# Optimization experiments

Hardware: AMD Instinct MI355X
Metric: run time of the kernel (lower is better)

## Reference

```python
import jax, jax.numpy as jnp
import numpy as np

N = 50000   # nodes
E = 800000  # edges per relation (avg degree 16)
IN = 128    # input feature dim
H = 2       # attention heads per layer
OUT = 64    # output feats per head
R = 2       # number of relations
NEG_SLOPE = 0.2


def _edge_softmax(e, dst, n):
    # e: [E, H] edge scores; softmax over incoming edges of each dst node
    m = jax.ops.segment_max(e, dst, num_segments=n)  # [N, H]
    m = jnp.where(jnp.isfinite(m), m, 0.0)
    ex = jnp.exp(e - jax.lax.stop_gradient(m)[dst])
    s = jax.ops.segment_sum(ex, dst, num_segments=n)  # [N, H]
    return ex / s[dst]


def _gat_layer(h, W, al, ar, b, src, dst):
    # h: [N, in]; W: [R, in, H*OUT]; al/ar: [R, H, OUT]; b: [R, H*OUT]
    # src/dst: [R, E] int32. HeteroGraphConv with sum aggregation over relations.
    acc = jnp.zeros((N, H, OUT), h.dtype)
    for r in range(R):  # small fixed relation count
        f = (h @ W[r]).reshape(N, H, OUT)           # projected feats
        el = (f * al[r]).sum(-1)                    # [N, H]
        er = (f * ar[r]).sum(-1)                    # [N, H]
        e = jax.nn.leaky_relu(el[src[r]] + er[dst[r]], NEG_SLOPE)  # [E, H]
        a = _edge_softmax(e, dst[r], N)             # [E, H]
        msg = f[src[r]] * a[:, :, None]             # [E, H, OUT]
        agg = jax.ops.segment_sum(msg, dst[r], num_segments=N)     # [N, H, OUT]
        acc = acc + jax.nn.elu(agg + b[r].reshape(1, H, OUT))
    return acc.reshape(N, H * OUT)  # flatten(1)


def setup_inputs() -> dict:
    key = jax.random.key(0)
    k = jax.random.split(key, 13)
    s = 0.05
    f32 = jnp.float32
    return {
        "x": jax.random.normal(k[0], (N, IN), f32),
        "W0": jax.random.normal(k[1], (R, IN, H * OUT), f32) * s,
        "al0": jax.random.normal(k[2], (R, H, OUT), f32) * s,
        "ar0": jax.random.normal(k[3], (R, H, OUT), f32) * s,
        "b0": jax.random.normal(k[4], (R, H * OUT), f32) * s,
        "W1": jax.random.normal(k[5], (R, H * OUT, H * OUT), f32) * s,
        "al1": jax.random.normal(k[6], (R, H, OUT), f32) * s,
        "ar1": jax.random.normal(k[7], (R, H, OUT), f32) * s,
        "b1": jax.random.normal(k[8], (R, H * OUT), f32) * s,
        "src0": jax.random.randint(k[9], (R, E), 0, N, jnp.int32),
        "dst0": jax.random.randint(k[10], (R, E), 0, N, jnp.int32),
        "src1": jax.random.randint(k[11], (R, E), 0, N, jnp.int32),
        "dst1": jax.random.randint(k[12], (R, E), 0, N, jnp.int32),
    }


def reference(x, W0, al0, ar0, b0, W1, al1, ar1, b1, src0, dst0, src1, dst1):
    h = _gat_layer(x, W0, al0, ar0, b0, src0, dst0)  # [N, H*OUT]
    h = _gat_layer(h, W1, al1, ar1, b1, src1, dst1)  # [N, H*OUT]
    return h
```

## Files before the change

kernel.cpp:

```cpp
#include <hip/hip_runtime.h>

#define NN 50000
#define NE 800000
#define DIM 128
#define NB 128
#define CH 4096
#define CAP 8192

typedef unsigned int uint;
typedef unsigned short ushort;
typedef __attribute__((ext_vector_type(8))) short v8s;
typedef __attribute__((ext_vector_type(4))) float v4f;

__device__ __forceinline__ ushort f2bf(float f) {
    union { float f; uint i; } c; c.f = f;
    const uint r = (c.i + 0x7fffu + ((c.i >> 16) & 1u)) >> 16;
    return (ushort)r;
}

__global__ __launch_bounds__(256) void conv_wt(
    const float* __restrict__ W0, const float* __restrict__ W1,
    ushort* __restrict__ WT)
{
    const int t = blockIdx.x * 256 + threadIdx.x;
#pragma unroll
    for (int i = 0; i < 4; i++) {
        const int o = t * 4 + i;
        const int m = o >> 14, rem = o & 16383;
        const int nrow = rem >> 7, k = rem & 127;
        const float* src = (m < 2) ? (W0 + (size_t)m * 16384)
                                   : (W1 + (size_t)(m - 2) * 16384);
        WT[o] = f2bf(src[k * 128 + nrow]);
    }
}

__global__ __launch_bounds__(256) void gemm_dual(
    const ushort* __restrict__ hbf, const float* __restrict__ xf,
    const ushort* __restrict__ WT,
    const float* __restrict__ al, const float* __restrict__ ar,
    ushort* __restrict__ fg0, ushort* __restrict__ fg1,
    float* __restrict__ elb, int n, int is_f32)
{
    __shared__ ushort tile[64][136];
    const int tid = threadIdx.x;
    const int w = tid >> 6, lane = tid & 63;
    const int quad = lane >> 4, l16 = lane & 15;
    const int row0 = blockIdx.x * 64 + w * 16;

    int arow = row0 + l16;
    if (arow >= n) arow = n - 1;

    v8s afr[4];
    if (is_f32) {
        const float* ap = xf + (size_t)arow * DIM + quad * 8;
#pragma unroll
        for (int kt = 0; kt < 4; kt++) {
            const float4 a0 = *(const float4*)(ap + kt * 32);
            const float4 a1 = *(const float4*)(ap + kt * 32 + 4);
            ushort tmp[8] = { f2bf(a0.x), f2bf(a0.y), f2bf(a0.z), f2bf(a0.w),
                              f2bf(a1.x), f2bf(a1.y), f2bf(a1.z), f2bf(a1.w) };
            afr[kt] = *(const v8s*)tmp;
        }
    } else {
        const ushort* ap = hbf + (size_t)arow * DIM + quad * 8;
#pragma unroll
        for (int kt = 0; kt < 4; kt++) afr[kt] = *(const v8s*)(ap + kt * 32);
    }

    for (int rel = 0; rel < 2; rel++) {
        const ushort* bp = WT + (size_t)rel * DIM * DIM + (size_t)l16 * DIM + quad * 8;
        v4f acc[8];
#pragma unroll
        for (int nt = 0; nt < 8; nt++) acc[nt] = (v4f)0.0f;
#pragma unroll
        for (int kt = 0; kt < 4; kt++) {
#pragma unroll
            for (int nt = 0; nt < 8; nt++) {
                const v8s b = *(const v8s*)(bp + (size_t)nt * 16 * DIM + kt * 32);
                acc[nt] = __builtin_amdgcn_mfma_f32_16x16x32_bf16(afr[kt], b, acc[nt], 0, 0, 0);
            }
        }

        const float* alr = al + rel * DIM;
        const float* arr = ar + rel * DIM;
        float pel[4][2], per2[4][2];
#pragma unroll
        for (int r = 0; r < 4; r++)
            pel[r][0] = pel[r][1] = per2[r][0] = per2[r][1] = 0.f;
#pragma unroll
        for (int nt = 0; nt < 8; nt++) {
            const int col = nt * 16 + l16;
            const float av = alr[col], rv = arr[col];
            const int head = nt >> 2;
#pragma unroll
            for (int r = 0; r < 4; r++) {
                pel[r][head] += acc[nt][r] * av;
                per2[r][head] += acc[nt][r] * rv;
            }
        }
#pragma unroll
        for (int o = 1; o < 16; o <<= 1) {
#pragma unroll
            for (int r = 0; r < 4; r++) {
#pragma unroll
                for (int h = 0; h < 2; h++) {
                    pel[r][h] += __shfl_xor(pel[r][h], o);
                    per2[r][h] += __shfl_xor(per2[r][h], o);
                }
            }
        }
        float* elp = elb + (size_t)rel * NN * 4;
        float* erp = elp + (size_t)NN * 2;
        if (l16 == 0) {
#pragma unroll
            for (int r = 0; r < 4; r++) {
                const int row = row0 + quad * 4 + r;
                if (row < n) {
#pragma unroll
                    for (int h = 0; h < 2; h++) {
                        elp[row * 2 + h] = pel[r][h];
                        erp[row * 2 + h] = per2[r][h];
                    }
                }
            }
        }

        __syncthreads();
        const int lr0 = w * 16 + quad * 4;
#pragma unroll
        for (int nt = 0; nt < 8; nt++) {
            const int col = nt * 16 + l16;
#pragma unroll
            for (int r = 0; r < 4; r++)
                tile[lr0 + r][col] = f2bf(acc[nt][r]);
        }
        __syncthreads();
        ushort* fgr = rel ? fg1 : fg0;
        const int srow = tid >> 2, ch = tid & 3;
        const int grow = blockIdx.x * 64 + srow;
        if (grow < n) {
            const uint4* lp = (const uint4*)&tile[srow][ch * 32];
            uint4* gp = (uint4*)(fgr + (size_t)grow * DIM + ch * 32);
            gp[0] = lp[0];
            gp[1] = lp[1];
            gp[2] = lp[2];
            gp[3] = lp[3];
        }
    }
}

__global__ __launch_bounds__(512) void init_gcur(int* __restrict__ gcur)
{
    const int i = threadIdx.x;
    gcur[i] = i * CAP;
}

__global__ __launch_bounds__(256) void bin_edges(
    const int* __restrict__ dst0, const int* __restrict__ dst1,
    const int* __restrict__ src0, const int* __restrict__ src1,
    int* __restrict__ gcur, uint* __restrict__ binned)
{
    __shared__ int hist[NB], ebase[NB], lcur[NB], gbase[NB], sc[NB];
    __shared__ uint stage[CH];
    const int bpset = (NE + CH - 1) / CH;
    const int bid = blockIdx.x;
    const int s = bid / bpset, cb = bid - s * bpset;
    const int* dstp = (s < 2) ? (dst0 + (size_t)s * NE) : (dst1 + (size_t)(s - 2) * NE);
    const int* srcp = (s < 2) ? (src0 + (size_t)s * NE) : (src1 + (size_t)(s - 2) * NE);
    const int e0 = cb * CH;
    const int t = threadIdx.x;

    if (t < NB) hist[t] = 0;
    __syncthreads();

    int myd[16], mys[16];
#pragma unroll
    for (int k = 0; k < 16; k++) {
        const int e = e0 + t + k * 256;
        if (e < NE) {
            const int d = dstp[e];
            myd[k] = d;
            mys[k] = srcp[e];
            atomicAdd(&hist[(d * NB) / NN], 1);
        } else myd[k] = -1;
    }
    __syncthreads();
    if (t < NB) sc[t] = hist[t];
    __syncthreads();
    for (int o = 1; o < NB; o <<= 1) {
        int tv = 0;
        if (t < NB && t >= o) tv = sc[t - o];
        __syncthreads();
        if (t < NB) sc[t] += tv;
        __syncthreads();
    }
    if (t < NB) {
        ebase[t] = sc[t] - hist[t];
        lcur[t]  = sc[t] - hist[t];
        gbase[t] = atomicAdd(&gcur[s * NB + t], hist[t]);
    }
    __syncthreads();
#pragma unroll
    for (int k = 0; k < 16; k++) {
        if (myd[k] >= 0) {
            const int b = (myd[k] * NB) / NN;
            const int p = atomicAdd(&lcur[b], 1);
            stage[p] = ((uint)myd[k] << 16) | (uint)mys[k];
        }
    }
    __syncthreads();
    const int total = ebase[NB - 1] + hist[NB - 1];
    for (int i = t; i < total; i += 256) {
        const uint v = stage[i];
        const int b = ((int)(v >> 16) * NB) / NN;
        binned[gbase[b] + (i - ebase[b])] = v;
    }
}

__global__ __launch_bounds__(64) void scan_buckets(
    const int* __restrict__ gcur, int* __restrict__ bbase, int* __restrict__ row)
{
    const int s = threadIdx.x;
    if (s < 4) {
        int acc = 0;
        for (int b = 0; b < NB; b++) {
            bbase[s * (NB + 1) + b] = acc;
            acc += gcur[s * NB + b] - (s * NB + b) * CAP;
        }
        bbase[s * (NB + 1) + NB] = acc;
        row[s * (NN + 1) + NN] = NE;
    }
}

__global__ __launch_bounds__(256) void build_csr(
    const int* __restrict__ bbase, const uint* __restrict__ binned,
    int* __restrict__ row, ushort* __restrict__ csr_src)
{
    __shared__ int A[512], B[512], lcur[512];
    const int bid = blockIdx.x;
    const int s = bid >> 7, b = bid & (NB - 1);
    const int nb0 = (b * NN + NB - 1) / NB;
    int nb1 = ((b + 1) * NN + NB - 1) / NB;
    if (nb1 > NN) nb1 = NN;
    const int nloc = nb1 - nb0;
    const int jb = bbase[s * (NB + 1) + b], je = bbase[s * (NB + 1) + b + 1];
    const int cnt = je - jb;
    const uint* bslot = binned + (size_t)(s * NB + b) * CAP;
    const int t = threadIdx.x;

    A[t] = 0; A[t + 256] = 0;
    __syncthreads();
    for (int j = t; j < cnt; j += 256)
        atomicAdd(&A[(int)(bslot[j] >> 16) - nb0], 1);
    __syncthreads();
    const int c0 = A[t], c1 = A[t + 256];
    int* cur = A; int* nxt = B;
    for (int off = 1; off < 512; off <<= 1) {
        nxt[t]       = cur[t]       + ((t >= off)       ? cur[t - off]       : 0);
        nxt[t + 256] = cur[t + 256] + ((t + 256 >= off) ? cur[t + 256 - off] : 0);
        __syncthreads();
        int* tmp = cur; cur = nxt; nxt = tmp;
    }
    if (t < nloc) {
        const int v = jb + cur[t] - c0;
        lcur[t] = v;
        row[s * (NN + 1) + nb0 + t] = v;
    }
    if (t + 256 < nloc) {
        const int v = jb + cur[t + 256] - c1;
        lcur[t + 256] = v;
        row[s * (NN + 1) + nb0 + t + 256] = v;
    }
    __syncthreads();
    ushort* outp = csr_src + (size_t)s * NE;
    for (int j = t; j < cnt; j += 256) {
        const uint v = bslot[j];
        const int p = atomicAdd(&lcur[(int)(v >> 16) - nb0], 1);
        outp[p] = (ushort)(v & 0xffffu);
    }
}

__device__ __forceinline__ float elu(float v) { return v > 0.f ? v : expm1f(v); }
__device__ __forceinline__ float2 bfpair(uint u) {
    union { uint i; float f; } lo, hi;
    lo.i = u << 16;
    hi.i = u & 0xffff0000u;
    return make_float2(lo.f, hi.f);
}

__global__ __launch_bounds__(256) void aggregate_dual(
    const int* __restrict__ row0, const ushort* __restrict__ csr0,
    const int* __restrict__ row1, const ushort* __restrict__ csr1,
    const float2* __restrict__ el0, const float2* __restrict__ er0,
    const float2* __restrict__ el1, const float2* __restrict__ er1,
    const ushort* __restrict__ fg0, const ushort* __restrict__ fg1,
    const float* __restrict__ bias0, const float* __restrict__ bias1,
    float* __restrict__ outf, ushort* __restrict__ outbf, int obf)
{
    __shared__ uint soff[4][64];
    __shared__ float wts[4][2][64];
    const int wv = (blockIdx.x * 256 + threadIdx.x) >> 6;
    if (wv >= NN) return;
    const int lane = threadIdx.x & 63;
    const int wid = threadIdx.x >> 6;

    const int* rows[2] = {row0, row1};
    const ushort* csrs[2] = {csr0, csr1};
    const float2* els[2] = {el0, el1};
    const float2* ers[2] = {er0, er1};
    const ushort* fgs[2] = {fg0, fg1};
    const float* biases[2] = {bias0, bias1};

    float oacc0 = 0.f, oacc1 = 0.f;

#pragma unroll
    for (int rel = 0; rel < 2; rel++) {
        const int beg = rows[rel][wv], end = rows[rel][wv + 1];
        const int deg = end - beg;
        const float2 erd = ers[rel][wv];
        float2 acc = make_float2(0.f, 0.f);

        if (deg <= 64) {
            uint sof = 0;
            float ex0 = 0.f, ex1 = 0.f;
            if (lane < deg) {
                const int s = csrs[rel][beg + lane];
                const float2 e = els[rel][s];
                float e0 = e.x + erd.x, e1 = e.y + erd.y;
                e0 = e0 > 0.f ? e0 : 0.2f * e0;
                e1 = e1 > 0.f ? e1 : 0.2f * e1;
                ex0 = __expf(e0);
                ex1 = __expf(e1);
                sof = (uint)s << 8;
            }
            float den0 = ex0, den1 = ex1;
            for (int o = 32; o > 0; o >>= 1) {
                den0 += __shfl_xor(den0, o);
                den1 += __shfl_xor(den1, o);
            }
            const float inv0 = 1.0f / den0, inv1 = 1.0f / den1;
            soff[wid][lane] = sof;
            wts[wid][0][lane] = ex0 * inv0;
            wts[wid][1][lane] = ex1 * inv1;
            const char* fgb = (const char*)fgs[rel] + lane * 4;
            const float* wrow = wts[wid][lane >> 5];
            const uint* sorow = soff[wid];
            int tt = 0;
            for (; tt + 4 <= deg; tt += 4) {
                const uint o0 = sorow[tt],     o1 = sorow[tt + 1];
                const uint o2 = sorow[tt + 2], o3 = sorow[tt + 3];
                const float w0 = wrow[tt],     w1 = wrow[tt + 1];
                const float w2 = wrow[tt + 2], w3 = wrow[tt + 3];
                const uint u0 = *(const uint*)(fgb + o0);
                const uint u1 = *(const uint*)(fgb + o1);
                const uint u2 = *(const uint*)(fgb + o2);
                const uint u3 = *(const uint*)(fgb + o3);
                const float2 f0 = bfpair(u0), f1 = bfpair(u1);
                const float2 f2 = bfpair(u2), f3 = bfpair(u3);
                acc.x += f0.x * w0 + f1.x * w1 + f2.x * w2 + f3.x * w3;
                acc.y += f0.y * w0 + f1.y * w1 + f2.y * w2 + f3.y * w3;
            }
            for (; tt < deg; tt++) {
                const uint o0 = sorow[tt];
                const float w0 = wrow[tt];
                const float2 f0 = bfpair(*(const uint*)(fgb + o0));
                acc.x += f0.x * w0;
                acc.y += f0.y * w0;
            }
        } else {
            float den0 = 0.f, den1 = 0.f;
            for (int c0 = beg; c0 < end; c0 += 64) {
                const int j = c0 + lane;
                if (j < end) {
                    const float2 e = els[rel][csrs[rel][j]];
                    float e0 = e.x + erd.x, e1 = e.y + erd.y;
                    e0 = e0 > 0.f ? e0 : 0.2f * e0;
                    e1 = e1 > 0.f ? e1 : 0.2f * e1;
                    den0 += __expf(e0);
                    den1 += __expf(e1);
                }
            }
            for (int o = 32; o > 0; o >>= 1) {
                den0 += __shfl_xor(den0, o);
                den1 += __shfl_xor(den1, o);
            }
            const float inv0 = 1.0f / den0, inv1 = 1.0f / den1;
            for (int c0 = beg; c0 < end; c0 += 64) {
                const int j = c0 + lane;
                int s = -1;
                float ex0 = 0.f, ex1 = 0.f;
                if (j < end) {
                    s = csrs[rel][j];
                    const float2 e = els[rel][s];
                    float e0 = e.x + erd.x, e1 = e.y + erd.y;
                    e0 = e0 > 0.f ? e0 : 0.2f * e0;
                    e1 = e1 > 0.f ? e1 : 0.2f * e1;
                    ex0 = __expf(e0) * inv0;
                    ex1 = __expf(e1) * inv1;
                }
                const int cm = min(64, end - c0);
                for (int tt = 0; tt < cm; tt++) {
                    const int st = __shfl(s, tt);
                    const float a0 = __shfl(ex0, tt);
                    const float a1 = __shfl(ex1, tt);
                    const float aa = (lane < 32) ? a0 : a1;
                    const float2 fv = bfpair(
                        *(const uint*)((const char*)fgs[rel] + ((size_t)st << 8) + lane * 4));
                    acc.x += fv.x * aa;
                    acc.y += fv.y * aa;
                }
            }
        }

        const float b0 = biases[rel][2 * lane], b1 = biases[rel][2 * lane + 1];
        oacc0 += elu(acc.x + b0);
        oacc1 += elu(acc.y + b1);
    }

    if (obf) {
        ushort tmp[2] = { f2bf(oacc0), f2bf(oacc1) };
        *(uint*)(outbf + (size_t)wv * DIM + 2 * lane) = *(const uint*)tmp;
    } else {
        float* op = outf + (size_t)wv * DIM + 2 * lane;
        op[0] = oacc0; op[1] = oacc1;
    }
}

extern "C" void kernel_launch(void* const* d_in, const int* in_sizes, int n_in,
                              void* d_out, int out_size, void* d_ws, size_t ws_size,
                              hipStream_t stream)
{
    const float* x   = (const float*)d_in[0];
    const float* W0  = (const float*)d_in[1];
    const float* al0 = (const float*)d_in[2];
    const float* ar0 = (const float*)d_in[3];
    const float* b0  = (const float*)d_in[4];
    const float* W1  = (const float*)d_in[5];
    const float* al1 = (const float*)d_in[6];
    const float* ar1 = (const float*)d_in[7];
    const float* b1  = (const float*)d_in[8];
    const int* src0 = (const int*)d_in[9];
    const int* dst0 = (const int*)d_in[10];
    const int* src1 = (const int*)d_in[11];
    const int* dst1 = (const int*)d_in[12];
    float* out = (float*)d_out;

    char* w = (char*)d_ws;
    auto alloc = [&](size_t bytes) {
        char* p = w; w += (bytes + 255) & ~(size_t)255; return p;
    };
    ushort* h1bf   = (ushort*)alloc((size_t)NN * DIM * 2);
    ushort* fg0    = (ushort*)alloc((size_t)NN * DIM * 2);
    ushort* fg1    = (ushort*)alloc((size_t)NN * DIM * 2);
    ushort* WT     = (ushort*)alloc((size_t)4 * DIM * DIM * 2);
    float*  elb    = (float*)alloc((size_t)8 * NN * 4);
    int*    row    = (int*)alloc((size_t)4 * (NN + 1) * 4);
    ushort* csr    = (ushort*)alloc((size_t)4 * NE * 2);
    uint*   binned = (uint*)alloc((size_t)4 * NB * CAP * 4);
    int*    bbase  = (int*)alloc((size_t)4 * (NB + 1) * 4);
    int*    gcur   = (int*)alloc((size_t)4 * NB * 4);

    conv_wt<<<64, 256, 0, stream>>>(W0, W1, WT);
    init_gcur<<<1, 512, 0, stream>>>(gcur);
    {
        const int bpset = (NE + CH - 1) / CH;
        bin_edges<<<4 * bpset, 256, 0, stream>>>(dst0, dst1, src0, src1, gcur, binned);
    }
    scan_buckets<<<1, 64, 0, stream>>>(gcur, bbase, row);
    build_csr<<<4 * NB, 256, 0, stream>>>(bbase, binned, row, csr);

    const int gblocks = (NN + 63) / 64;
    for (int L = 0; L < 2; L++) {
        const ushort* WTl = WT + (size_t)L * 2 * DIM * DIM;
        const float* al  = L ? al1 : al0;
        const float* ar  = L ? ar1 : ar0;
        const float* b   = L ? b1 : b0;
        gemm_dual<<<gblocks, 256, 0, stream>>>(
            L ? h1bf : nullptr, L ? nullptr : x, WTl, al, ar,
            fg0, fg1, elb, NN, L ? 0 : 1);
        const int es0 = L * 2, es1 = L * 2 + 1;
        float* el0p = elb;
        float* er0p = elb + (size_t)NN * 2;
        float* el1p = elb + (size_t)NN * 4;
        float* er1p = elb + (size_t)NN * 6;
        aggregate_dual<<<(NN * 64 + 255) / 256, 256, 0, stream>>>(
            row + es0 * (NN + 1), csr + (size_t)es0 * NE,
            row + es1 * (NN + 1), csr + (size_t)es1 * NE,
            (const float2*)el0p, (const float2*)er0p,
            (const float2*)el1p, (const float2*)er1p,
            fg0, fg1, b, b + DIM,
            L ? out : nullptr, L ? nullptr : h1bf, L ? 0 : 1);
    }
}
```

Baseline: 373.2 us.

## Split edge gather across half-waves with 8-byte loads and packed LDS entries

Each half of the 64-lane wave now handles alternating edges (even or odd). Each lane loads 4 bf16 features (8 bytes) instead of 2, and the two halves' partial sums are combined with a cross-half shuffle before bias and ELU. Source offset and attention weight are packed into a single uint2 LDS entry per edge and head. The high-degree path also switches from per-edge shuffle broadcasts to the same LDS-based loop. The aim is fewer gather instructions per edge and fewer LDS reads, at the cost of an extra reduction step and only half the lanes doing the final store.

```diff
diff --git a/kernel.cpp b/kernel.cpp
--- a/kernel.cpp
+++ b/kernel.cpp
@@ -297,8 +297,7 @@
     const float* __restrict__ bias0, const float* __restrict__ bias1,
     float* __restrict__ outf, ushort* __restrict__ outbf, int obf)
 {
-    __shared__ uint soff[4][64];
-    __shared__ float wts[4][2][64];
+    __shared__ uint2 wo[4][2][64];
     const int wv = (blockIdx.x * 256 + threadIdx.x) >> 6;
     if (wv >= NN) return;
     const int lane = threadIdx.x & 63;
@@ -311,14 +310,20 @@
     const ushort* fgs[2] = {fg0, fg1};
     const float* biases[2] = {bias0, bias1};
 
-    float oacc0 = 0.f, oacc1 = 0.f;
+    const uint laneoff = (uint)(lane & 31) * 8u;
+    const int head = (lane >> 4) & 1;
+    const int half = lane >> 5;
+
+    float4 o4 = make_float4(0.f, 0.f, 0.f, 0.f);
 
 #pragma unroll
     for (int rel = 0; rel < 2; rel++) {
         const int beg = rows[rel][wv], end = rows[rel][wv + 1];
         const int deg = end - beg;
         const float2 erd = ers[rel][wv];
-        float2 acc = make_float2(0.f, 0.f);
+        const char* fgb = (const char*)fgs[rel];
+        const uint2* wop = &wo[wid][head][half];
+        float4 a4 = make_float4(0.f, 0.f, 0.f, 0.f);
 
         if (deg <= 64) {
             uint sof = 0;
@@ -339,33 +344,17 @@
                 den1 += __shfl_xor(den1, o);
             }
             const float inv0 = 1.0f / den0, inv1 = 1.0f / den1;
-            soff[wid][lane] = sof;
-            wts[wid][0][lane] = ex0 * inv0;
-            wts[wid][1][lane] = ex1 * inv1;
-            const char* fgb = (const char*)fgs[rel] + lane * 4;
-            const float* wrow = wts[wid][lane >> 5];
-            const uint* sorow = soff[wid];
-            int tt = 0;
-            for (; tt + 4 <= deg; tt += 4) {
-                const uint o0 = sorow[tt],     o1 = sorow[tt + 1];
-                const uint o2 = sorow[tt + 2], o3 = sorow[tt + 3];
-                const float w0 = wrow[tt],     w1 = wrow[tt + 1];
-                const float w2 = wrow[tt + 2], w3 = wrow[tt + 3];
-                const uint u0 = *(const uint*)(fgb + o0);
-                const uint u1 = *(const uint*)(fgb + o1);
-                const uint u2 = *(const uint*)(fgb + o2);
-                const uint u3 = *(const uint*)(fgb + o3);
-                const float2 f0 = bfpair(u0), f1 = bfpair(u1);
-                const float2 f2 = bfpair(u2), f3 = bfpair(u3);
-                acc.x += f0.x * w0 + f1.x * w1 + f2.x * w2 + f3.x * w3;
-                acc.y += f0.y * w0 + f1.y * w1 + f2.y * w2 + f3.y * w3;
-            }
-            for (; tt < deg; tt++) {
-                const uint o0 = sorow[tt];
-                const float w0 = wrow[tt];
-                const float2 f0 = bfpair(*(const uint*)(fgb + o0));
-                acc.x += f0.x * w0;
-                acc.y += f0.y * w0;
+            wo[wid][0][lane] = make_uint2(sof, __float_as_uint(ex0 * inv0));
+            wo[wid][1][lane] = make_uint2(sof, __float_as_uint(ex1 * inv1));
+            const int dp = (deg + 1) & ~1;
+#pragma unroll 4
+            for (int tt = 0; tt < dp; tt += 2) {
+                const uint2 ow = wop[tt];
+                const float wgt = __uint_as_float(ow.y);
+                const uint2 u = *(const uint2*)(fgb + (ow.x + laneoff));
+                const float2 lo = bfpair(u.x), hi = bfpair(u.y);
+                a4.x += lo.x * wgt; a4.y += lo.y * wgt;
+                a4.z += hi.x * wgt; a4.w += hi.y * wgt;
             }
         } else {
             float den0 = 0.f, den1 = 0.f;
@@ -387,42 +376,52 @@
             const float inv0 = 1.0f / den0, inv1 = 1.0f / den1;
             for (int c0 = beg; c0 < end; c0 += 64) {
                 const int j = c0 + lane;
-                int s = -1;
-                float ex0 = 0.f, ex1 = 0.f;
+                uint sof = 0;
+                float w0 = 0.f, w1 = 0.f;
                 if (j < end) {
-                    s = csrs[rel][j];
+                    const int s = csrs[rel][j];
                     const float2 e = els[rel][s];
                     float e0 = e.x + erd.x, e1 = e.y + erd.y;
                     e0 = e0 > 0.f ? e0 : 0.2f * e0;
                     e1 = e1 > 0.f ? e1 : 0.2f * e1;
-                    ex0 = __expf(e0) * inv0;
-                    ex1 = __expf(e1) * inv1;
+                    w0 = __expf(e0) * inv0;
+                    w1 = __expf(e1) * inv1;
+                    sof = (uint)s << 8;
                 }
-                const int cm = min(64, end - c0);
-                for (int tt = 0; tt < cm; tt++) {
-                    const int st = __shfl(s, tt);
-                    const float a0 = __shfl(ex0, tt);
-                    const float a1 = __shfl(ex1, tt);
-                    const float aa = (lane < 32) ? a0 : a1;
-                    const float2 fv = bfpair(
-                        *(const uint*)((const char*)fgs[rel] + ((size_t)st << 8) + lane * 4));
-                    acc.x += fv.x * aa;
-                    acc.y += fv.y * aa;
+                wo[wid][0][lane] = make_uint2(sof, __float_as_uint(w0));
+                wo[wid][1][lane] = make_uint2(sof, __float_as_uint(w1));
+                const int cl = min(64, end - c0);
+                const int dp = (cl + 1) & ~1;
+                for (int tt = 0; tt < dp; tt += 2) {
+                    const uint2 ow = wop[tt];
+                    const float wgt = __uint_as_float(ow.y);
+                    const uint2 u = *(const uint2*)(fgb + (ow.x + laneoff));
+                    const float2 lo = bfpair(u.x), hi = bfpair(u.y);
+                    a4.x += lo.x * wgt; a4.y += lo.y * wgt;
+                    a4.z += hi.x * wgt; a4.w += hi.y * wgt;
                 }
             }
         }
 
-        const float b0 = biases[rel][2 * lane], b1 = biases[rel][2 * lane + 1];
-        oacc0 += elu(acc.x + b0);
-        oacc1 += elu(acc.y + b1);
-    }
-
-    if (obf) {
-        ushort tmp[2] = { f2bf(oacc0), f2bf(oacc1) };
-        *(uint*)(outbf + (size_t)wv * DIM + 2 * lane) = *(const uint*)tmp;
-    } else {
-        float* op = outf + (size_t)wv * DIM + 2 * lane;
-        op[0] = oacc0; op[1] = oacc1;
+        a4.x += __shfl_xor(a4.x, 32);
+        a4.y += __shfl_xor(a4.y, 32);
+        a4.z += __shfl_xor(a4.z, 32);
+        a4.w += __shfl_xor(a4.w, 32);
+
+        const float4 bv = *(const float4*)(biases[rel] + 4 * (lane & 31));
+        o4.x += elu(a4.x + bv.x);
+        o4.y += elu(a4.y + bv.y);
+        o4.z += elu(a4.z + bv.z);
+        o4.w += elu(a4.w + bv.w);
+    }
+
+    if (lane < 32) {
+        if (obf) {
+            ushort tmp[4] = { f2bf(o4.x), f2bf(o4.y), f2bf(o4.z), f2bf(o4.w) };
+            *(uint2*)(outbf + (size_t)wv * DIM + 4 * lane) = *(const uint2*)tmp;
+        } else {
+            *(float4*)(outf + (size_t)wv * DIM + 4 * lane) = o4;
+        }
     }
 }
 
```

New measurement: 366.9 us. Within noise of the previous version (-1.7%).
